# Performance work log

Measured on AMD Instinct MI355X. Metric: run time of the kernel, lower is better.

Reference implementation:

```python
import jax, jax.numpy as jnp
import numpy as np

DIM = 1024
HEADS = 16
HDIM = DIM // HEADS
HIDDEN = 4 * DIM
SCALE = HDIM ** -0.5


def layernorm(x, g, b, eps=1e-5):
    mu = jnp.mean(x, axis=-1, keepdims=True)
    var = jnp.var(x, axis=-1, keepdims=True)
    return (x - mu) * jax.lax.rsqrt(var + eps) * g + b


def setup_inputs() -> dict:
    key = jax.random.key(0)
    ks = jax.random.split(key, 8)
    s = 0.02
    return {
        "x": jax.random.normal(ks[0], (4, 1024, DIM), dtype=jnp.float32),
        "ln1_g": jnp.ones((DIM,), jnp.float32),
        "ln1_b": jnp.zeros((DIM,), jnp.float32),
        "ln2_g": jnp.ones((DIM,), jnp.float32),
        "ln2_b": jnp.zeros((DIM,), jnp.float32),
        "qkv_w": jax.random.normal(ks[1], (DIM, 3 * DIM), jnp.float32) * s,
        "qkv_b": jnp.zeros((3 * DIM,), jnp.float32),
        "proj_w": jax.random.normal(ks[2], (DIM, DIM), jnp.float32) * s,
        "proj_b": jnp.zeros((DIM,), jnp.float32),
        "fc1_w": jax.random.normal(ks[3], (DIM, HIDDEN), jnp.float32) * s,
        "fc1_b": jnp.zeros((HIDDEN,), jnp.float32),
        "fc2_w": jax.random.normal(ks[4], (HIDDEN, DIM), jnp.float32) * s,
        "fc2_b": jnp.zeros((DIM,), jnp.float32),
    }


def reference(x, ln1_g, ln1_b, ln2_g, ln2_b, qkv_w, qkv_b, proj_w, proj_b,
              fc1_w, fc1_b, fc2_w, fc2_b):
    B, N, C = x.shape
    # --- attention branch ---
    h = layernorm(x, ln1_g, ln1_b)
    qkv = h @ qkv_w + qkv_b                       # [B,N,3C]
    qkv = qkv.reshape(B, N, 3, HEADS, HDIM)
    q, k, v = jnp.moveaxis(qkv, 2, 0)             # each [B,N,H,Dh]
    q = jnp.swapaxes(q, 1, 2)                      # [B,H,N,Dh]
    k = jnp.swapaxes(k, 1, 2)
    v = jnp.swapaxes(v, 1, 2)
    attn = jnp.einsum('bhqd,bhkd->bhqk', q, k) * SCALE
    attn = jax.nn.softmax(attn, axis=-1)
    o = jnp.einsum('bhqk,bhkd->bhqd', attn, v)     # [B,H,N,Dh]
    o = jnp.swapaxes(o, 1, 2).reshape(B, N, C)
    x = x + (o @ proj_w + proj_b)
    # --- MLP branch ---
    h = layernorm(x, ln2_g, ln2_b)
    h = jax.nn.gelu(h @ fc1_w + fc1_b, approximate=False)
    x = x + (h @ fc2_w + fc2_b)
    return x
```

## Files before the change

kernel.cpp:

```cpp
#include <hip/hip_runtime.h>
#include <math.h>

#define DIM    1024
#define HEADS  16
#define HDIM   64
#define HIDDEN 4096
#define BATCH  4
#define SEQ    1024
#define ROWS   (BATCH * SEQ)

typedef short s16x8 __attribute__((ext_vector_type(8)));
typedef float f32x4 __attribute__((ext_vector_type(4)));

__device__ __forceinline__ float blo(unsigned int u) {
    union { unsigned int i; float f; } x; x.i = u << 16; return x.f;
}
__device__ __forceinline__ float bhi(unsigned int u) {
    union { unsigned int i; float f; } x; x.i = u & 0xffff0000u; return x.f;
}
__device__ __forceinline__ unsigned short f2b(float f) {
    union { float f; unsigned int i; } x; x.f = f;
    unsigned int r = x.i + 0x7fffu + ((x.i >> 16) & 1u);
    return (unsigned short)(r >> 16);
}

__device__ __forceinline__ float gelu_f(float x) {
    float z  = fabsf(x) * 0.70710678118f;
    float t  = __builtin_amdgcn_rcpf(__builtin_fmaf(0.3275911f, z, 1.0f));
    float p  = ((((1.061405429f * t - 1.453152027f) * t + 1.421413741f) * t
                 - 0.284496736f) * t + 0.254829592f) * t;
    float e  = exp2f(-0.72134752f * x * x);
    float w  = 0.5f * p * e;
    float phi = (x >= 0.0f) ? (1.0f - w) : w;
    return x * phi;
}

__device__ __forceinline__ size_t tidx(int row, int k, int Kdim) {
    return ((size_t)(row >> 4) * (Kdim >> 5) + (k >> 5)) * 512
         + (size_t)(((k & 31) >> 3) * 128 + (row & 15) * 8 + (k & 7));
}

__device__ __forceinline__ void gload_lds16(const void* g, void* l) {
    __builtin_amdgcn_global_load_lds(
        (const __attribute__((address_space(1))) unsigned int*)g,
        (__attribute__((address_space(3))) unsigned int*)l, 16, 0, 0);
}

__global__ __launch_bounds__(256) void prep_kernel(const float* __restrict__ x,
                                                   const float* __restrict__ g,
                                                   const float* __restrict__ b,
                                                   unsigned short* __restrict__ lnout,
                                                   const float* __restrict__ qkv_w,
                                                   unsigned short* __restrict__ wT_qkv,
                                                   const float* __restrict__ proj_w,
                                                   unsigned short* __restrict__ wT_proj,
                                                   const float* __restrict__ fc1_w,
                                                   unsigned short* __restrict__ wT_fc1,
                                                   const float* __restrict__ fc2_w,
                                                   unsigned short* __restrict__ wT_fc2) {
    __shared__ float red1[256], red2[256];
    __shared__ unsigned short T[64][68];
    const int bid = blockIdx.x;
    const int t = threadIdx.x;

    if (bid < ROWS) {
        int row = bid;
        const float* xr = x + (size_t)row * DIM;
        float4 v = *((const float4*)(xr + t * 4));
        float s  = v.x + v.y + v.z + v.w;
        float ss = v.x * v.x + v.y * v.y + v.z * v.z + v.w * v.w;
        red1[t] = s; red2[t] = ss;
        __syncthreads();
        for (int off = 128; off > 0; off >>= 1) {
            if (t < off) { red1[t] += red1[t + off]; red2[t] += red2[t + off]; }
            __syncthreads();
        }
        float mu   = red1[0] * (1.0f / DIM);
        float var  = red2[0] * (1.0f / DIM) - mu * mu;
        float rstd = rsqrtf(var + 1e-5f);
        float4 gv = *((const float4*)(g + t * 4));
        float4 bv = *((const float4*)(b + t * 4));
        ushort4 o;
        o.x = f2b((v.x - mu) * rstd * gv.x + bv.x);
        o.y = f2b((v.y - mu) * rstd * gv.y + bv.y);
        o.z = f2b((v.z - mu) * rstd * gv.z + bv.z);
        o.w = f2b((v.w - mu) * rstd * gv.w + bv.w);
        *((ushort4*)(lnout + tidx(row, t * 4, DIM))) = o;
    } else {
        int tt = bid - ROWS;
        const float* W; unsigned short* Wt; int K, N, bx, by;
        if (tt < 768) {
            W = qkv_w; Wt = wT_qkv; K = DIM; N = 3 * DIM; bx = tt % 48; by = tt / 48;
        } else if (tt < 768 + 256) {
            tt -= 768;
            W = proj_w; Wt = wT_proj; K = DIM; N = DIM; bx = tt % 16; by = tt / 16;
        } else if (tt < 768 + 256 + 1024) {
            tt -= 768 + 256;
            W = fc1_w; Wt = wT_fc1; K = DIM; N = HIDDEN; bx = tt % 64; by = tt / 64;
        } else {
            tt -= 768 + 256 + 1024;
            W = fc2_w; Wt = wT_fc2; K = HIDDEN; N = DIM; bx = tt % 16; by = tt / 16;
        }
        int n0 = bx * 64, k0 = by * 64;
        int cr = t >> 4;
        int cc = (t & 15) * 4;
        #pragma unroll
        for (int r = 0; r < 4; ++r) {
            int kk = cr + 16 * r;
            float4 v = *((const float4*)(W + (size_t)(k0 + kk) * N + n0 + cc));
            T[cc + 0][kk] = f2b(v.x);
            T[cc + 1][kk] = f2b(v.y);
            T[cc + 2][kk] = f2b(v.z);
            T[cc + 3][kk] = f2b(v.w);
        }
        __syncthreads();
        {
            int nn = t >> 2;
            int kg = (t & 3) * 16;
            #pragma unroll
            for (int p = 0; p < 2; ++p) {
                int k8 = kg + p * 8;
                ushort4 lo = *((ushort4*)&T[nn][k8]);
                ushort4 hi = *((ushort4*)&T[nn][k8 + 4]);
                unsigned short* dst = Wt + tidx(n0 + nn, k0 + k8, K);
                *((ushort4*)dst)       = lo;
                *((ushort4*)(dst + 4)) = hi;
            }
        }
    }
}

__global__ __launch_bounds__(256) void reduce_ln(const unsigned short* __restrict__ p0,
                                                 const unsigned short* __restrict__ p1,
                                                 const float* __restrict__ x,
                                                 const float* __restrict__ bias,
                                                 const float* __restrict__ g,
                                                 const float* __restrict__ b,
                                                 float* __restrict__ xout,
                                                 unsigned short* __restrict__ lnout) {
    int row = blockIdx.x;
    int t = threadIdx.x;
    size_t i = (size_t)row * DIM + t * 4;
    float4 xv = *((const float4*)(x + i));
    float4 bi = *((const float4*)(bias + t * 4));
    uint2 w0 = *((const uint2*)(p0 + i));
    uint2 w1 = *((const uint2*)(p1 + i));
    float4 v;
    v.x = xv.x + bi.x + blo(w0.x) + blo(w1.x);
    v.y = xv.y + bi.y + bhi(w0.x) + bhi(w1.x);
    v.z = xv.z + bi.z + blo(w0.y) + blo(w1.y);
    v.w = xv.w + bi.w + bhi(w0.y) + bhi(w1.y);
    *((float4*)(xout + i)) = v;

    float s  = v.x + v.y + v.z + v.w;
    float ss = v.x * v.x + v.y * v.y + v.z * v.z + v.w * v.w;
    __shared__ float red1[256], red2[256];
    red1[t] = s; red2[t] = ss;
    __syncthreads();
    for (int off = 128; off > 0; off >>= 1) {
        if (t < off) { red1[t] += red1[t + off]; red2[t] += red2[t + off]; }
        __syncthreads();
    }
    float mu   = red1[0] * (1.0f / DIM);
    float var  = red2[0] * (1.0f / DIM) - mu * mu;
    float rstd = rsqrtf(var + 1e-5f);
    float4 gv = *((const float4*)(g + t * 4));
    float4 bv = *((const float4*)(b + t * 4));
    ushort4 o;
    o.x = f2b((v.x - mu) * rstd * gv.x + bv.x);
    o.y = f2b((v.y - mu) * rstd * gv.y + bv.y);
    o.z = f2b((v.z - mu) * rstd * gv.z + bv.z);
    o.w = f2b((v.w - mu) * rstd * gv.w + bv.w);
    *((ushort4*)(lnout + tidx(row, t * 4, DIM))) = o;
}

__global__ __launch_bounds__(256, 4) void mfma_gemm(const unsigned short* __restrict__ A,
                                                 const unsigned short* __restrict__ Bt,
                                                 const float* __restrict__ bias,
                                                 void* __restrict__ Cout,
                                                 unsigned short* __restrict__ vt,
                                                 unsigned short* __restrict__ p0,
                                                 unsigned short* __restrict__ p1,
                                                 unsigned short* __restrict__ p2,
                                                 unsigned short* __restrict__ p3,
                                                 int M, int N, int K, int Ksplit, int fuse) {
    __shared__ __align__(16) short Asm[8192];
    __shared__ __align__(16) short Bsm[8192];

    const int tid  = threadIdx.x;
    const int lane = tid & 63;
    const int wave = tid >> 6;
    const int wy = wave >> 1, wx = wave & 1;
    const int lr = lane & 15;
    const int lq = lane >> 4;

    int m_t, n_t;
    {
        const int mt = gridDim.x, ntl = gridDim.y, G = 8;
        if (ntl > G) {
            int lin = blockIdx.y * mt + blockIdx.x;
            int gsz = mt * G;
            int grp = lin / gsz;
            int rem = lin - grp * gsz;
            m_t = rem % mt;
            n_t = grp * G + rem / mt;
        } else { m_t = blockIdx.x; n_t = blockIdx.y; }
    }
    const int m0 = m_t * 128, n0 = n_t * 128;
    const int kbase = blockIdx.z * Ksplit;
    const int kch = K >> 5;

    f32x4 acc[4][4];
    #pragma unroll
    for (int i = 0; i < 4; ++i)
        #pragma unroll
        for (int j = 0; j < 4; ++j)
            acc[i][j] = (f32x4){0.f, 0.f, 0.f, 0.f};

    const unsigned short* ag[4]; const unsigned short* bg[4];
    short* al[4]; short* bl[4];
    #pragma unroll
    for (int j = 0; j < 4; ++j) {
        int cid = wave * 4 + j;
        int mb  = cid >> 1;
        int kc  = cid & 1;
        ag[j] = A  + ((size_t)((m0 >> 4) + mb) * kch + (kbase >> 5) + kc) * 512 + lane * 8;
        bg[j] = Bt + ((size_t)((n0 >> 4) + mb) * kch + (kbase >> 5) + kc) * 512 + lane * 8;
        al[j] = &Asm[cid * 512];
        bl[j] = &Bsm[cid * 512];
    }

    for (int k0 = 0; k0 < Ksplit; k0 += 64) {
        #pragma unroll
        for (int j = 0; j < 4; ++j) {
            gload_lds16(ag[j], al[j]);
            gload_lds16(bg[j], bl[j]);
            ag[j] += 1024; bg[j] += 1024;
        }
        __syncthreads();
        #pragma unroll
        for (int kc = 0; kc < 2; ++kc) {
            s16x8 af[4], bf[4];
            #pragma unroll
            for (int i = 0; i < 4; ++i)
                af[i] = *((const s16x8*)&Asm[((wy * 4 + i) * 2 + kc) * 512 + lane * 8]);
            #pragma unroll
            for (int j = 0; j < 4; ++j)
                bf[j] = *((const s16x8*)&Bsm[((wx * 4 + j) * 2 + kc) * 512 + lane * 8]);
            #pragma unroll
            for (int i = 0; i < 4; ++i)
                #pragma unroll
                for (int j = 0; j < 4; ++j)
                    acc[i][j] = __builtin_amdgcn_mfma_f32_16x16x32_bf16(af[i], bf[j], acc[i][j], 0, 0, 0);
        }
        __syncthreads();
    }

    short* Wl = (wave < 2 ? Asm : Bsm) + (wave & 1) * 4096;

    if (fuse == 0 && vt && (n0 + wx * 64) >= 2 * DIM) {
        #pragma unroll
        for (int j = 0; j < 4; ++j) {
            int col = n0 + wx * 64 + j * 16 + lr;
            float bi = bias[col];
            #pragma unroll
            for (int i = 0; i < 4; ++i) {
                int row0 = m0 + wy * 64 + i * 16 + lq * 4;
                #pragma unroll
                for (int r = 0; r < 4; ++r) {
                    float val = acc[i][j][r] + bi;
                    int row = row0 + r;
                    int b_ = row >> 10, tok = row & 1023;
                    int hd = col - 2 * DIM, h_ = hd >> 6, d = hd & 63;
                    size_t o = (size_t)(b_ * 16 + h_) * 65536
                             + ((size_t)(d >> 4) * 32 + (tok >> 5)) * 512
                             + ((tok & 31) >> 3) * 128 + (d & 15) * 8 + (tok & 7);
                    vt[o] = f2b(val);
                }
            }
        }
    } else if (fuse == 3) {
        #pragma unroll
        for (int j = 0; j < 4; ++j) {
            #pragma unroll
            for (int i = 0; i < 4; ++i) {
                #pragma unroll
                for (int r = 0; r < 4; ++r) {
                    int rowL = i * 16 + lq * 4 + r;
                    int colL = (j * 16 + lr) ^ ((rowL & 7) << 3);
                    Wl[rowL * 64 + colL] = (short)f2b(acc[i][j][r]);
                }
            }
        }
        int z = blockIdx.z;
        unsigned short* P = (z == 0) ? p0 : (z == 1) ? p1 : (z == 2) ? p2 : p3;
        unsigned short* Prow = P + (size_t)(m0 + wy * 64 + lane) * N + n0 + wx * 64;
        #pragma unroll
        for (int c = 0; c < 8; ++c) {
            int colr = (c * 8) ^ ((lane & 7) << 3);
            s16x8 v = *((const s16x8*)&Wl[lane * 64 + colr]);
            *((s16x8*)&Prow[c * 8]) = v;
        }
    } else {
        #pragma unroll
        for (int j = 0; j < 4; ++j) {
            float bi = bias[n0 + wx * 64 + j * 16 + lr];
            #pragma unroll
            for (int i = 0; i < 4; ++i) {
                #pragma unroll
                for (int r = 0; r < 4; ++r) {
                    float val = acc[i][j][r] + bi;
                    if (fuse == 1) val = gelu_f(val);
                    int colL = (j & 1) * 16 + lr;
                    int hi = colL >> 3;
                    int pos = hi * 128 + (lq * 4 + r) * 8 + (lr & 7);
                    pos ^= ((pos >> 7) & 3) << 3;
                    Wl[(i * 2 + (j >> 1)) * 512 + pos] = (short)f2b(val);
                }
            }
        }
        const size_t rc0 = (size_t)((m0 + wy * 64) >> 4);
        const size_t cc0 = (size_t)((n0 + wx * 64) >> 5);
        const size_t nch = (size_t)(N >> 5);
        #pragma unroll
        for (int c = 0; c < 8; ++c) {
            int raddr = lane * 8;
            raddr ^= ((raddr >> 7) & 3) << 3;
            s16x8 v = *((const s16x8*)&Wl[c * 512 + raddr]);
            size_t chunk = (rc0 + (c >> 1)) * nch + cc0 + (c & 1);
            *((s16x8*)&((unsigned short*)Cout)[chunk * 512 + lane * 8]) = v;
        }
    }
}

__global__ __launch_bounds__(256) void reduce_kernel(const unsigned short* __restrict__ p0,
                                                     const unsigned short* __restrict__ p1,
                                                     const unsigned short* __restrict__ p2,
                                                     const unsigned short* __restrict__ p3,
                                                     int S,
                                                     const float* __restrict__ x,
                                                     const float* __restrict__ bias,
                                                     float* __restrict__ out) {
    int i = (blockIdx.x * 256 + threadIdx.x) * 8;
    int col = i & (DIM - 1);
    float4 b0 = *((const float4*)(bias + col));
    float4 b1 = *((const float4*)(bias + col + 4));
    float4 x0 = *((const float4*)(x + i));
    float4 x1 = *((const float4*)(x + i + 4));
    float a[8] = {x0.x + b0.x, x0.y + b0.y, x0.z + b0.z, x0.w + b0.w,
                  x1.x + b1.x, x1.y + b1.y, x1.z + b1.z, x1.w + b1.w};
    const unsigned short* ps[4] = {p0, p1, p2, p3};
    for (int s = 0; s < S; ++s) {
        uint4 w = *((const uint4*)(ps[s] + i));
        a[0] += blo(w.x); a[1] += bhi(w.x);
        a[2] += blo(w.y); a[3] += bhi(w.y);
        a[4] += blo(w.z); a[5] += bhi(w.z);
        a[6] += blo(w.w); a[7] += bhi(w.w);
    }
    *((float4*)(out + i))     = make_float4(a[0], a[1], a[2], a[3]);
    *((float4*)(out + i + 4)) = make_float4(a[4], a[5], a[6], a[7]);
}

__global__ __launch_bounds__(256) void fattn_mfma(const unsigned short* __restrict__ qkv,
                                                  const unsigned short* __restrict__ Vt,
                                                  unsigned short* __restrict__ out) {
    __shared__ __align__(16) short Qs[8192];
    __shared__ __align__(16) short Ks[4096];
    __shared__ __align__(16) short Vs[4096];
    __shared__ __align__(16) short Ps[128 * 72];
    __shared__ __align__(16) short OnesB[512];

    const int tid = threadIdx.x, lane = tid & 63, wave = tid >> 6;
    const int lr = lane & 15, lq = lane >> 4;
    const int L = blockIdx.x;
    const int bh = (L & 7) + 8 * (L >> 6);
    const int b = bh >> 4, h = bh & 15;
    const int q0 = ((L >> 3) & 7) * 128;

    {
        s16x8 z = (s16x8){0,0,0,0,0,0,0,0};
        if (lr == 0) { z[0] = (short)0x3F80; z[1] = (short)0x3F80;
                       z[2] = (short)0x3F80; z[3] = (short)0x3F80;
                       z[4] = (short)0x3F80; z[5] = (short)0x3F80;
                       z[6] = (short)0x3F80; z[7] = (short)0x3F80; }
        if (wave == 0) *((s16x8*)&OnesB[lane * 8]) = z;
    }

    #pragma unroll
    for (int j = 0; j < 4; ++j) {
        int cid = wave * 4 + j;
        const unsigned short* g = qkv + ((size_t)(((b * SEQ + q0) >> 4) + (cid >> 1)) * 96
                                         + 2 * h + (cid & 1)) * 512 + lane * 8;
        gload_lds16(g, &Qs[cid * 512]);
    }

    const unsigned short* kg_[2]; const unsigned short* vg_[2];
    short *kl_[2], *vl_[2];
    #pragma unroll
    for (int j = 0; j < 2; ++j) {
        int cid = wave * 2 + j;
        kg_[j] = qkv + ((size_t)(((b * SEQ) >> 4) + (cid >> 1)) * 96
                        + 32 + 2 * h + (cid & 1)) * 512 + lane * 8;
        vg_[j] = Vt + (size_t)bh * 65536
                 + ((size_t)(cid >> 1) * 32 + (cid & 1)) * 512 + lane * 8;
        kl_[j] = &Ks[cid * 512];
        vl_[j] = &Vs[cid * 512];
    }

    f32x4 osum[2][5];
    #pragma unroll
    for (int i = 0; i < 2; ++i)
        #pragma unroll
        for (int d = 0; d < 5; ++d)
            osum[i][d] = (f32x4){0.f, 0.f, 0.f, 0.f};

    const float c = 0.125f * 1.44269504f;

    for (int k0 = 0; k0 < SEQ; k0 += 64) {
        #pragma unroll
        for (int j = 0; j < 2; ++j) {
            gload_lds16(kg_[j], kl_[j]);
            gload_lds16(vg_[j], vl_[j]);
            kg_[j] += 4 * 96 * 512;
            vg_[j] += 1024;
        }
        __syncthreads();

        f32x4 s[2][4];
        #pragma unroll
        for (int i = 0; i < 2; ++i)
            #pragma unroll
            for (int jb = 0; jb < 4; ++jb)
                s[i][jb] = (f32x4){0.f, 0.f, 0.f, 0.f};
        #pragma unroll
        for (int kc = 0; kc < 2; ++kc) {
            s16x8 aq0 = *((const s16x8*)&Qs[(wave * 4 + 0 + kc) * 512 + lane * 8]);
            s16x8 aq1 = *((const s16x8*)&Qs[(wave * 4 + 2 + kc) * 512 + lane * 8]);
            #pragma unroll
            for (int jb = 0; jb < 4; ++jb) {
                s16x8 bk = *((const s16x8*)&Ks[(jb * 2 + kc) * 512 + lane * 8]);
                s[0][jb] = __builtin_amdgcn_mfma_f32_16x16x32_bf16(aq0, bk, s[0][jb], 0, 0, 0);
                s[1][jb] = __builtin_amdgcn_mfma_f32_16x16x32_bf16(aq1, bk, s[1][jb], 0, 0, 0);
            }
        }

        #pragma unroll
        for (int i = 0; i < 2; ++i)
            #pragma unroll
            for (int r = 0; r < 4; ++r) {
                int prow = (wave * 2 + i) * 16 + lq * 4 + r;
                #pragma unroll
                for (int jb = 0; jb < 4; ++jb)
                    Ps[prow * 72 + jb * 16 + lr] = (short)f2b(exp2f(s[i][jb][r] * c));
            }

        #pragma unroll
        for (int kc = 0; kc < 2; ++kc) {
            s16x8 ap0 = *((const s16x8*)&Ps[((wave * 2 + 0) * 16 + lr) * 72 + kc * 32 + lq * 8]);
            s16x8 ap1 = *((const s16x8*)&Ps[((wave * 2 + 1) * 16 + lr) * 72 + kc * 32 + lq * 8]);
            #pragma unroll
            for (int db = 0; db < 4; ++db) {
                s16x8 bv = *((const s16x8*)&Vs[(db * 2 + kc) * 512 + lane * 8]);
                osum[0][db] = __builtin_amdgcn_mfma_f32_16x16x32_bf16(ap0, bv, osum[0][db], 0, 0, 0);
                osum[1][db] = __builtin_amdgcn_mfma_f32_16x16x32_bf16(ap1, bv, osum[1][db], 0, 0, 0);
            }
            s16x8 bo = *((const s16x8*)&OnesB[lane * 8]);
            osum[0][4] = __builtin_amdgcn_mfma_f32_16x16x32_bf16(ap0, bo, osum[0][4], 0, 0, 0);
            osum[1][4] = __builtin_amdgcn_mfma_f32_16x16x32_bf16(ap1, bo, osum[1][4], 0, 0, 0);
        }
        __syncthreads();
    }

    #pragma unroll
    for (int i = 0; i < 2; ++i) {
        int qrow = q0 + (wave * 2 + i) * 16 + lq * 4;
        #pragma unroll
        for (int r = 0; r < 4; ++r) {
            float lsum = __shfl(osum[i][4][r], lane & 48, 64);
            float inv = 1.0f / lsum;
            int row = b * SEQ + qrow + r;
            #pragma unroll
            for (int db = 0; db < 4; ++db)
                out[tidx(row, h * 64 + db * 16 + lr, DIM)] = f2b(osum[i][db][r] * inv);
        }
    }
}

extern "C" void kernel_launch(void* const* d_in, const int* in_sizes, int n_in,
                              void* d_out, int out_size, void* d_ws, size_t ws_size,
                              hipStream_t stream) {
    const float* x      = (const float*)d_in[0];
    const float* ln1_g  = (const float*)d_in[1];
    const float* ln1_b  = (const float*)d_in[2];
    const float* ln2_g  = (const float*)d_in[3];
    const float* ln2_b  = (const float*)d_in[4];
    const float* qkv_w  = (const float*)d_in[5];
    const float* qkv_b  = (const float*)d_in[6];
    const float* proj_w = (const float*)d_in[7];
    const float* proj_b = (const float*)d_in[8];
    const float* fc1_w  = (const float*)d_in[9];
    const float* fc1_b  = (const float*)d_in[10];
    const float* fc2_w  = (const float*)d_in[11];
    const float* fc2_b  = (const float*)d_in[12];
    float* out = (float*)d_out;

    char* ws = (char*)d_ws;
    unsigned short* wT_fc2  = (unsigned short*)(ws);
    unsigned short* wT_qkv  = (unsigned short*)(ws + (8u  << 20));
    unsigned short* wT_proj = (unsigned short*)(ws + (14u << 20));
    unsigned short* qkvbuf  = (unsigned short*)(ws + (16u << 20));
    unsigned short* Vt      = (unsigned short*)(ws + (40u << 20));
    unsigned short* attnout = (unsigned short*)(ws + (48u << 20));
    unsigned short* lnout   = (unsigned short*)(ws + (56u << 20));
    unsigned short* wT_fc1  = (unsigned short*)(ws + (64u << 20));
    unsigned short* gelu    = (unsigned short*)(ws + (16u << 20));
    unsigned short* pp0 = (unsigned short*)(ws + (16u << 20));
    unsigned short* pp1 = (unsigned short*)(ws + (24u << 20));
    unsigned short* fp0 = (unsigned short*)(ws + (48u << 20));
    unsigned short* fp1 = (unsigned short*)(ws + (56u << 20));
    unsigned short* fp2 = (unsigned short*)(ws + (64u << 20));
    unsigned short* fp3 = (unsigned short*)(ws + (8u  << 20));

    prep_kernel<<<ROWS + 3072, 256, 0, stream>>>(
        x, ln1_g, ln1_b, lnout,
        qkv_w, wT_qkv, proj_w, wT_proj, fc1_w, wT_fc1, fc2_w, wT_fc2);
    mfma_gemm<<<dim3(ROWS / 128, 3 * DIM / 128, 1), 256, 0, stream>>>(
        lnout, wT_qkv, qkv_b, qkvbuf, Vt, nullptr, nullptr, nullptr, nullptr,
        ROWS, 3 * DIM, DIM, DIM, 0);
    fattn_mfma<<<(SEQ / 128) * BATCH * HEADS, 256, 0, stream>>>(qkvbuf, Vt, attnout);
    mfma_gemm<<<dim3(ROWS / 128, DIM / 128, 2), 256, 0, stream>>>(
        attnout, wT_proj, proj_b, nullptr, nullptr, pp0, pp1, nullptr, nullptr,
        ROWS, DIM, DIM, DIM / 2, 3);
    reduce_ln<<<ROWS, 256, 0, stream>>>(pp0, pp1, x, proj_b, ln2_g, ln2_b, out, lnout);
    mfma_gemm<<<dim3(ROWS / 128, HIDDEN / 128, 1), 256, 0, stream>>>(
        lnout, wT_fc1, fc1_b, gelu, nullptr, nullptr, nullptr, nullptr, nullptr,
        ROWS, HIDDEN, DIM, DIM, 1);
    mfma_gemm<<<dim3(ROWS / 128, DIM / 128, 4), 256, 0, stream>>>(
        gelu, wT_fc2, fc2_b, nullptr, nullptr, fp0, fp1, fp2, fp3,
        ROWS, DIM, HIDDEN, HIDDEN / 4, 3);
    reduce_kernel<<<ROWS * DIM / 2048, 256, 0, stream>>>(
        fp0, fp1, fp2, fp3, 4, out, fc2_b, out);
}
```

Measured before the change: 328.4 us.

## Double-buffer GEMM LDS loads and fuse fc2 residual epilogue, dropping split-K reduce

The GEMM main loop now keeps two LDS buffers, issuing the next K-tile's global-to-LDS loads while MFMAs run on the current one. Launch bounds drop from 4 to 2 blocks per SM to fit the doubled shared memory. The fc2 GEMM no longer uses 4-way split-K with bf16 partials and a separate reduce kernel. It runs full-K and adds bias plus the residual in an fp32 epilogue staged through LDS. The partial-sum traffic and one launch go away, at the cost of fewer blocks (256) for fc2 and lower occupancy.

```diff
diff --git a/kernel.cpp b/kernel.cpp
--- a/kernel.cpp
+++ b/kernel.cpp
@@ -174,18 +174,17 @@
     *((ushort4*)(lnout + tidx(row, t * 4, DIM))) = o;
 }
 
-__global__ __launch_bounds__(256, 4) void mfma_gemm(const unsigned short* __restrict__ A,
+__global__ __launch_bounds__(256, 2) void mfma_gemm(const unsigned short* __restrict__ A,
                                                  const unsigned short* __restrict__ Bt,
                                                  const float* __restrict__ bias,
+                                                 const float* __restrict__ add,
                                                  void* __restrict__ Cout,
                                                  unsigned short* __restrict__ vt,
                                                  unsigned short* __restrict__ p0,
                                                  unsigned short* __restrict__ p1,
-                                                 unsigned short* __restrict__ p2,
-                                                 unsigned short* __restrict__ p3,
                                                  int M, int N, int K, int Ksplit, int fuse) {
-    __shared__ __align__(16) short Asm[8192];
-    __shared__ __align__(16) short Bsm[8192];
+    __shared__ __align__(16) short Asm[2][8192];
+    __shared__ __align__(16) short Bsm[2][8192];
 
     const int tid  = threadIdx.x;
     const int lane = tid & 63;
@@ -218,7 +217,6 @@
             acc[i][j] = (f32x4){0.f, 0.f, 0.f, 0.f};
 
     const unsigned short* ag[4]; const unsigned short* bg[4];
-    short* al[4]; short* bl[4];
     #pragma unroll
     for (int j = 0; j < 4; ++j) {
         int cid = wave * 4 + j;
@@ -226,37 +224,40 @@
         int kc  = cid & 1;
         ag[j] = A  + ((size_t)((m0 >> 4) + mb) * kch + (kbase >> 5) + kc) * 512 + lane * 8;
         bg[j] = Bt + ((size_t)((n0 >> 4) + mb) * kch + (kbase >> 5) + kc) * 512 + lane * 8;
-        al[j] = &Asm[cid * 512];
-        bl[j] = &Bsm[cid * 512];
-    }
-
-    for (int k0 = 0; k0 < Ksplit; k0 += 64) {
-        #pragma unroll
-        for (int j = 0; j < 4; ++j) {
-            gload_lds16(ag[j], al[j]);
-            gload_lds16(bg[j], bl[j]);
-            ag[j] += 1024; bg[j] += 1024;
-        }
-        __syncthreads();
-        #pragma unroll
-        for (int kc = 0; kc < 2; ++kc) {
-            s16x8 af[4], bf[4];
-            #pragma unroll
-            for (int i = 0; i < 4; ++i)
-                af[i] = *((const s16x8*)&Asm[((wy * 4 + i) * 2 + kc) * 512 + lane * 8]);
-            #pragma unroll
-            for (int j = 0; j < 4; ++j)
-                bf[j] = *((const s16x8*)&Bsm[((wx * 4 + j) * 2 + kc) * 512 + lane * 8]);
-            #pragma unroll
-            for (int i = 0; i < 4; ++i)
-                #pragma unroll
-                for (int j = 0; j < 4; ++j)
-                    acc[i][j] = __builtin_amdgcn_mfma_f32_16x16x32_bf16(af[i], bf[j], acc[i][j], 0, 0, 0);
-        }
-        __syncthreads();
-    }
-
-    short* Wl = (wave < 2 ? Asm : Bsm) + (wave & 1) * 4096;
+    }
+
+#define STAGE(buf) { \
+    _Pragma("unroll") for (int j_ = 0; j_ < 4; ++j_) { \
+        gload_lds16(ag[j_], &Asm[buf][(wave * 4 + j_) * 512]); \
+        gload_lds16(bg[j_], &Bsm[buf][(wave * 4 + j_) * 512]); \
+        ag[j_] += 1024; bg[j_] += 1024; \
+    } }
+#define COMPUTE(buf) { \
+    _Pragma("unroll") for (int kc_ = 0; kc_ < 2; ++kc_) { \
+        s16x8 af[4], bf[4]; \
+        _Pragma("unroll") for (int i_ = 0; i_ < 4; ++i_) \
+            af[i_] = *((const s16x8*)&Asm[buf][((wy * 4 + i_) * 2 + kc_) * 512 + lane * 8]); \
+        _Pragma("unroll") for (int j_ = 0; j_ < 4; ++j_) \
+            bf[j_] = *((const s16x8*)&Bsm[buf][((wx * 4 + j_) * 2 + kc_) * 512 + lane * 8]); \
+        _Pragma("unroll") for (int i_ = 0; i_ < 4; ++i_) \
+            _Pragma("unroll") for (int j_ = 0; j_ < 4; ++j_) \
+                acc[i_][j_] = __builtin_amdgcn_mfma_f32_16x16x32_bf16(af[i_], bf[j_], acc[i_][j_], 0, 0, 0); \
+    } }
+
+    STAGE(0);
+    __syncthreads();
+    for (int k0 = 0; k0 < Ksplit; k0 += 128) {
+        STAGE(1);
+        COMPUTE(0);
+        __syncthreads();
+        if (k0 + 128 < Ksplit) STAGE(0);
+        COMPUTE(1);
+        __syncthreads();
+    }
+#undef STAGE
+#undef COMPUTE
+
+    short* Wl = (wave < 2 ? (short*)Asm : (short*)Bsm) + (wave & 1) * 4096;
 
     if (fuse == 0 && vt && (n0 + wx * 64) >= 2 * DIM) {
         #pragma unroll
@@ -279,6 +280,33 @@
                 }
             }
         }
+    } else if (fuse == 2) {
+        float* W32 = (float*)((wave < 2 ? (short*)Asm : (short*)Bsm) + (wave & 1) * 8192);
+        #pragma unroll
+        for (int j = 0; j < 4; ++j) {
+            float bi = bias[n0 + wx * 64 + j * 16 + lr];
+            #pragma unroll
+            for (int i = 0; i < 4; ++i) {
+                #pragma unroll
+                for (int r = 0; r < 4; ++r) {
+                    int rowL = i * 16 + lq * 4 + r;
+                    int colL = (j * 16 + lr) ^ ((rowL & 3) << 4);
+                    W32[rowL * 64 + colL] = acc[i][j][r] + bi;
+                }
+            }
+        }
+        float* orow = (float*)Cout + (size_t)(m0 + wy * 64) * N + n0 + wx * 64;
+        const float* arow = add + (size_t)(m0 + wy * 64) * N + n0 + wx * 64;
+        #pragma unroll
+        for (int pass = 0; pass < 16; ++pass) {
+            int rowL = pass * 4 + lq;
+            int pos = (lr * 4) ^ ((rowL & 3) << 4);
+            float4 v = *((float4*)&W32[rowL * 64 + pos]);
+            size_t off = (size_t)rowL * N + lr * 4;
+            float4 a = *((const float4*)&arow[off]);
+            v.x += a.x; v.y += a.y; v.z += a.z; v.w += a.w;
+            *((float4*)&orow[off]) = v;
+        }
     } else if (fuse == 3) {
         #pragma unroll
         for (int j = 0; j < 4; ++j) {
@@ -292,8 +320,7 @@
                 }
             }
         }
-        int z = blockIdx.z;
-        unsigned short* P = (z == 0) ? p0 : (z == 1) ? p1 : (z == 2) ? p2 : p3;
+        unsigned short* P = (blockIdx.z == 0) ? p0 : p1;
         unsigned short* Prow = P + (size_t)(m0 + wy * 64 + lane) * N + n0 + wx * 64;
         #pragma unroll
         for (int c = 0; c < 8; ++c) {
@@ -331,34 +358,6 @@
             *((s16x8*)&((unsigned short*)Cout)[chunk * 512 + lane * 8]) = v;
         }
     }
-}
-
-__global__ __launch_bounds__(256) void reduce_kernel(const unsigned short* __restrict__ p0,
-                                                     const unsigned short* __restrict__ p1,
-                                                     const unsigned short* __restrict__ p2,
-                                                     const unsigned short* __restrict__ p3,
-                                                     int S,
-                                                     const float* __restrict__ x,
-                                                     const float* __restrict__ bias,
-                                                     float* __restrict__ out) {
-    int i = (blockIdx.x * 256 + threadIdx.x) * 8;
-    int col = i & (DIM - 1);
-    float4 b0 = *((const float4*)(bias + col));
-    float4 b1 = *((const float4*)(bias + col + 4));
-    float4 x0 = *((const float4*)(x + i));
-    float4 x1 = *((const float4*)(x + i + 4));
-    float a[8] = {x0.x + b0.x, x0.y + b0.y, x0.z + b0.z, x0.w + b0.w,
-                  x1.x + b1.x, x1.y + b1.y, x1.z + b1.z, x1.w + b1.w};
-    const unsigned short* ps[4] = {p0, p1, p2, p3};
-    for (int s = 0; s < S; ++s) {
-        uint4 w = *((const uint4*)(ps[s] + i));
-        a[0] += blo(w.x); a[1] += bhi(w.x);
-        a[2] += blo(w.y); a[3] += bhi(w.y);
-        a[4] += blo(w.z); a[5] += bhi(w.z);
-        a[6] += blo(w.w); a[7] += bhi(w.w);
-    }
-    *((float4*)(out + i))     = make_float4(a[0], a[1], a[2], a[3]);
-    *((float4*)(out + i + 4)) = make_float4(a[4], a[5], a[6], a[7]);
 }
 
 __global__ __launch_bounds__(256) void fattn_mfma(const unsigned short* __restrict__ qkv,
@@ -516,28 +515,22 @@
     unsigned short* gelu    = (unsigned short*)(ws + (16u << 20));
     unsigned short* pp0 = (unsigned short*)(ws + (16u << 20));
     unsigned short* pp1 = (unsigned short*)(ws + (24u << 20));
-    unsigned short* fp0 = (unsigned short*)(ws + (48u << 20));
-    unsigned short* fp1 = (unsigned short*)(ws + (56u << 20));
-    unsigned short* fp2 = (unsigned short*)(ws + (64u << 20));
-    unsigned short* fp3 = (unsigned short*)(ws + (8u  << 20));
 
     prep_kernel<<<ROWS + 3072, 256, 0, stream>>>(
         x, ln1_g, ln1_b, lnout,
         qkv_w, wT_qkv, proj_w, wT_proj, fc1_w, wT_fc1, fc2_w, wT_fc2);
     mfma_gemm<<<dim3(ROWS / 128, 3 * DIM / 128, 1), 256, 0, stream>>>(
-        lnout, wT_qkv, qkv_b, qkvbuf, Vt, nullptr, nullptr, nullptr, nullptr,
+        lnout, wT_qkv, qkv_b, nullptr, qkvbuf, Vt, nullptr, nullptr,
         ROWS, 3 * DIM, DIM, DIM, 0);
     fattn_mfma<<<(SEQ / 128) * BATCH * HEADS, 256, 0, stream>>>(qkvbuf, Vt, attnout);
     mfma_gemm<<<dim3(ROWS / 128, DIM / 128, 2), 256, 0, stream>>>(
-        attnout, wT_proj, proj_b, nullptr, nullptr, pp0, pp1, nullptr, nullptr,
+        attnout, wT_proj, proj_b, nullptr, nullptr, nullptr, pp0, pp1,
         ROWS, DIM, DIM, DIM / 2, 3);
     reduce_ln<<<ROWS, 256, 0, stream>>>(pp0, pp1, x, proj_b, ln2_g, ln2_b, out, lnout);
     mfma_gemm<<<dim3(ROWS / 128, HIDDEN / 128, 1), 256, 0, stream>>>(
-        lnout, wT_fc1, fc1_b, gelu, nullptr, nullptr, nullptr, nullptr, nullptr,
+        lnout, wT_fc1, fc1_b, nullptr, gelu, nullptr, nullptr, nullptr,
         ROWS, HIDDEN, DIM, DIM, 1);
-    mfma_gemm<<<dim3(ROWS / 128, DIM / 128, 4), 256, 0, stream>>>(
-        gelu, wT_fc2, fc2_b, nullptr, nullptr, fp0, fp1, fp2, fp3,
-        ROWS, DIM, HIDDEN, HIDDEN / 4, 3);
-    reduce_kernel<<<ROWS * DIM / 2048, 256, 0, stream>>>(
-        fp0, fp1, fp2, fp3, 4, out, fc2_b, out);
-}
+    mfma_gemm<<<dim3(ROWS / 128, DIM / 128, 1), 256, 0, stream>>>(
+        gelu, wT_fc2, fc2_b, out, out, nullptr, nullptr, nullptr,
+        ROWS, DIM, HIDDEN, HIDDEN, 2);
+}
```

Measured after the change: 366.3 us. 11.6% more time.
